# Performance work log

Measured on AMD Instinct MI355X. Metric: run time of the kernel, lower is better.

Reference implementation:

```python
import jax, jax.numpy as jnp
import numpy as np

N_NODES = 50000
N_EDGES = 800000
IN_F, HID, OUT, FC_OUT = 192, 128, 64, 192


def setup_inputs() -> dict:
    key = jax.random.key(0)
    ks = jax.random.split(key, 12)
    s = 0.05
    return {
        "x": jax.random.normal(ks[0], (N_NODES, IN_F), dtype=jnp.float32),
        "edge_index": jax.random.randint(ks[1], (2, N_EDGES), 0, N_NODES, dtype=jnp.int64),
        "W1": jax.random.normal(ks[2], (IN_F, HID), dtype=jnp.float32) * s,
        "b1": jnp.zeros((HID,), jnp.float32),
        "Wg": jax.random.normal(ks[3], (HID, HID), dtype=jnp.float32) * s,
        "a_src": jax.random.normal(ks[4], (HID,), dtype=jnp.float32) * s,
        "a_dst": jax.random.normal(ks[5], (HID,), dtype=jnp.float32) * s,
        "bg": jnp.zeros((HID,), jnp.float32),
        "W2": jax.random.normal(ks[6], (HID, OUT), dtype=jnp.float32) * s,
        "b2": jnp.zeros((OUT,), jnp.float32),
        "Wf": jax.random.normal(ks[7], (OUT, FC_OUT), dtype=jnp.float32) * s,
        "bf": jnp.zeros((FC_OUT,), jnp.float32),
    }


def reference(x, edge_index, W1, b1, Wg, a_src, a_dst, bg, W2, b2, Wf, bf):
    N = x.shape[0]
    loops = jnp.arange(N, dtype=edge_index.dtype)
    src = jnp.concatenate([edge_index[0], loops])  # [E+N]
    dst = jnp.concatenate([edge_index[1], loops])

    # GCN symmetric normalization with self-loops (PyG gcn_norm)
    deg = jax.ops.segment_sum(jnp.ones_like(dst, dtype=x.dtype), dst, num_segments=N)
    dinv = jax.lax.rsqrt(jnp.maximum(deg, 1.0))  # deg >= 1 due to self-loops
    norm = dinv[src] * dinv[dst]  # [E+N]

    def gcn(h, W, b):
        h = h @ W
        out = jax.ops.segment_sum(h[src] * norm[:, None], dst, num_segments=N)
        return out + b

    h = gcn(x, W1, b1)  # [N, HID]

    # GAT layer (1 head, PyG defaults: self-loops, LeakyReLU(0.2), softmax over dst)
    hg = h @ Wg
    al = hg @ a_src  # [N]
    ar = hg @ a_dst  # [N]
    e = jax.nn.leaky_relu(al[src] + ar[dst], 0.2)  # [E+N]
    emax = jax.ops.segment_max(e, dst, num_segments=N)
    ex = jnp.exp(e - emax[dst])
    denom = jax.ops.segment_sum(ex, dst, num_segments=N)
    alpha = ex / denom[dst]
    h = jax.ops.segment_sum(hg[src] * alpha[:, None], dst, num_segments=N) + bg

    h = jax.nn.relu(h)
    h = gcn(h, W2, b2)  # [N, OUT]
    return h @ Wf + bf  # [N, 192]
```

## Files before the change

### kernel.cpp

```cpp
#include <hip/hip_runtime.h>
#include <hip/hip_fp16.h>
#include <cstdint>
#include <cstddef>

#define NN 50000
#define NE 800000
#define RNG 8
#define RSZ ((NN + RNG - 1) / RNG)
#define CPR 256
#define FILLB (RNG*CPR)

typedef _Float16 half8 __attribute__((ext_vector_type(8)));
typedef float    f32x4 __attribute__((ext_vector_type(4)));

static __device__ __forceinline__ float lrelu02(float x){ return x > 0.f ? x : 0.2f*x; }

static __device__ __forceinline__ float2 h2f(uint32_t u){
  __half2 h = *reinterpret_cast<__half2*>(&u);
  return __half22float2(h);
}
static __device__ __forceinline__ uint32_t f2h(float a, float b){
  __half2 h = __floats2half2_rn(a, b);
  return *reinterpret_cast<uint32_t*>(&h);
}
static __device__ __forceinline__ void acc8p(float* acc, uint4 raw, float p){
  float2 f0=h2f(raw.x), f1=h2f(raw.y), f2=h2f(raw.z), f3=h2f(raw.w);
  acc[0]+=p*f0.x; acc[1]+=p*f0.y; acc[2]+=p*f1.x; acc[3]+=p*f1.y;
  acc[4]+=p*f2.x; acc[5]+=p*f2.y; acc[6]+=p*f3.x; acc[7]+=p*f3.y;
}
static __device__ __forceinline__ void acc8s(float* acc, uint4 raw){
  float2 f0=h2f(raw.x), f1=h2f(raw.y), f2=h2f(raw.z), f3=h2f(raw.w);
  acc[0]+=f0.x; acc[1]+=f0.y; acc[2]+=f1.x; acc[3]+=f1.y;
  acc[4]+=f2.x; acc[5]+=f2.y; acc[6]+=f3.x; acc[7]+=f3.y;
}

__global__ __launch_bounds__(256) void pack_all_kernel(
    const float* __restrict__ W1, const float* __restrict__ Wg,
    const float* __restrict__ W2, const float* __restrict__ Wf,
    _Float16* __restrict__ B1, _Float16* __restrict__ B2,
    _Float16* __restrict__ B3, _Float16* __restrict__ B4,
    int* __restrict__ cnt)
{
  const int b = blockIdx.x;
  if (b >= 240){
    const int i = (b - 240)*256 + threadIdx.x;
    if (i < NN) cnt[i] = 0;
    return;
  }
  const float* B; _Float16* O; int K, N, base;
  if      (b < 96)  { B = W1; O = B1; K = 192; N = 128; base = 0;   }
  else if (b < 160) { B = Wg; O = B2; K = 128; N = 128; base = 96;  }
  else if (b < 192) { B = W2; O = B3; K = 128; N = 64;  base = 160; }
  else              { B = Wf; O = B4; K = 64;  N = 192; base = 192; }
  const int i = (b - base)*256 + threadIdx.x;
  if (i >= K*N) return;
  const int j    = i & 7;
  const int lane = (i >> 3) & 63;
  const int tile = i >> 9;
  const int ntl  = N >> 4;
  const int ct   = tile % ntl;
  const int k0   = (tile / ntl) << 5;
  const int k = k0 + ((lane >> 4) << 3) + j;
  const int n = (ct << 4) + (lane & 15);
  O[i] = (_Float16)B[(size_t)k*N + n];
}

__global__ __launch_bounds__(256) void count_kernel(const int* __restrict__ dst,
                                                    int* __restrict__ cnt, int E){
  const int r  = blockIdx.x % RNG;
  const int i  = blockIdx.x / RNG;
  const int lo = r * RSZ;
  const int hi = min(lo + RSZ, NN);
  const int cs = (E + CPR - 1) / CPR;
  const int e1 = min((i+1)*cs, E);
  for (int e = i*cs + threadIdx.x; e < e1; e += 256){
    const int d = dst[e];
    if (d >= lo && d < hi) atomicAdd(&cnt[d], 1);
  }
}

__global__ __launch_bounds__(1024) void scan1_kernel(const int* __restrict__ cnt,
      int* __restrict__ incl, int* __restrict__ bsum, int N){
  __shared__ int tmp[1024];
  const int t = threadIdx.x;
  const int i = blockIdx.x*1024 + t;
  int v = (i < N) ? cnt[i] : 0;
  tmp[t] = v;
  __syncthreads();
  #pragma unroll
  for (int off = 1; off < 1024; off <<= 1){
    int u = (t >= off) ? tmp[t-off] : 0;
    __syncthreads();
    tmp[t] += u;
    __syncthreads();
  }
  if (i < N) incl[i] = tmp[t];
  if (t == 1023) bsum[blockIdx.x] = tmp[t];
}

__global__ __launch_bounds__(256) void scan3_kernel(const int* __restrict__ cnt,
      const int* __restrict__ incl, const int* __restrict__ bsum,
      int* __restrict__ rp, int* __restrict__ fillp,
      float* __restrict__ dinv, int N, int NB){
  __shared__ int pre[64];
  const int t = threadIdx.x;
  if (t < 64){
    int own = (t < NB) ? bsum[t] : 0;
    int v = own;
    #pragma unroll
    for (int off = 1; off < 64; off <<= 1){
      int u = __shfl_up(v, off, 64);
      if (t >= off) v += u;
    }
    pre[t] = v - own;
  }
  __syncthreads();
  const int i = blockIdx.x*256 + t;
  if (i >= N) return;
  const int c = cnt[i];
  const int e = pre[i >> 10] + incl[i] - c;
  rp[i] = e; fillp[i] = e;
  dinv[i] = rsqrtf((float)(c + 1));
  if (i == N-1) rp[N] = e + c;
}

template<int K, int NT, bool AHALF, bool HALF_OUT, bool DOTS>
static __device__ __forceinline__ void gemm_block(
    const void* __restrict__ Av, const _Float16* __restrict__ Bsw,
    const float* __restrict__ bias, const float* __restrict__ rowscale,
    const float* __restrict__ avs, const float* __restrict__ avd,
    float* __restrict__ al, float* __restrict__ ar,
    void* __restrict__ Cv, int M, int N, int bm, int t)
{
  constexpr int NTL = NT*4;
  const int w    = t >> 6;
  const int lane = t & 63;
  const int m    = lane & 15;
  const int quad = lane >> 4;

  f32x4 acc[NTL];
  #pragma unroll
  for (int ct = 0; ct < NTL; ++ct) acc[ct] = (f32x4){0.f,0.f,0.f,0.f};

  const int row = bm + w*16 + m;
  const _Float16* bp = Bsw + lane*8;

  #pragma unroll
  for (int k0 = 0; k0 < K; k0 += 32){
    union { half8 h; uint4 u; uint32_t w[4]; } ua;
    if constexpr (AHALF){
      if (row < M){
        ua.u = *(const uint4*)((const _Float16*)Av + (size_t)row*K + k0 + quad*8);
      } else {
        ua.u = make_uint4(0u,0u,0u,0u);
      }
    } else {
      if (row < M){
        const float* Arow = (const float*)Av + (size_t)row*K;
        const float4 va = *(const float4*)(Arow + k0 + quad*8);
        const float4 vb = *(const float4*)(Arow + k0 + quad*8 + 4);
        ua.w[0] = f2h(va.x, va.y);
        ua.w[1] = f2h(va.z, va.w);
        ua.w[2] = f2h(vb.x, vb.y);
        ua.w[3] = f2h(vb.z, vb.w);
      } else {
        ua.u = make_uint4(0u,0u,0u,0u);
      }
    }
    const half8 af = ua.h;
    #pragma unroll
    for (int ct = 0; ct < NTL; ++ct){
      const half8 bf = *(const half8*)(bp + ((size_t)((k0>>5)*NTL + ct))*512);
      acc[ct] = __builtin_amdgcn_mfma_f32_16x16x32_f16(af, bf, acc[ct], 0, 0, 0);
    }
  }

  float rs[4];
  #pragma unroll
  for (int reg = 0; reg < 4; ++reg){
    const int r = bm + w*16 + quad*4 + reg;
    rs[reg] = (rowscale && r < M) ? rowscale[r] : 1.f;
  }
  float dal[4] = {0.f,0.f,0.f,0.f};
  float dar[4] = {0.f,0.f,0.f,0.f};
  #pragma unroll
  for (int ct = 0; ct < NTL; ++ct){
    const int colg = ct*16 + m;
    const float bv = bias ? bias[colg] : 0.f;
    float s_c = 0.f, d_c = 0.f;
    if constexpr (DOTS){ s_c = avs[colg]; d_c = avd[colg]; }
    #pragma unroll
    for (int reg = 0; reg < 4; ++reg){
      const int r = bm + w*16 + quad*4 + reg;
      if (r < M){
        const float v = rs[reg]*acc[ct][reg] + bv;
        if constexpr (DOTS){ dal[reg] += v*s_c; dar[reg] += v*d_c; }
        if constexpr (HALF_OUT){
          ((__half*)Cv)[(size_t)r*N + colg] = __float2half(v);
        } else {
          ((float*)Cv)[(size_t)r*N + colg] = v;
        }
      }
    }
  }
  if constexpr (DOTS){
    #pragma unroll
    for (int off = 1; off < 16; off <<= 1){
      #pragma unroll
      for (int reg = 0; reg < 4; ++reg){
        dal[reg] += __shfl_xor(dal[reg], off, 64);
        dar[reg] += __shfl_xor(dar[reg], off, 64);
      }
    }
    if (m == 0){
      #pragma unroll
      for (int reg = 0; reg < 4; ++reg){
        const int r = bm + w*16 + quad*4 + reg;
        if (r < M){
          al[r] = dal[reg];
          ar[r] = dar[reg];
        }
      }
    }
  }
}

template<int K, int NT, bool AHALF, bool HALF_OUT, bool DOTS>
__global__ __launch_bounds__(256) void gemm_mfma_kernel(
    const void* __restrict__ Av, const _Float16* __restrict__ Bsw,
    const float* __restrict__ bias, const float* __restrict__ rowscale,
    const float* __restrict__ avs, const float* __restrict__ avd,
    float* __restrict__ al, float* __restrict__ ar,
    void* __restrict__ Cv, int M, int N)
{
  gemm_block<K,NT,AHALF,HALF_OUT,DOTS>(Av, Bsw, bias, rowscale, avs, avd, al, ar,
                                       Cv, M, N, blockIdx.x*64, threadIdx.x);
}

__global__ __launch_bounds__(256) void fill_gemm1_kernel(
    const int* __restrict__ src, const int* __restrict__ dst,
    int* __restrict__ fillp, int* __restrict__ col, int E,
    const float* __restrict__ A, const _Float16* __restrict__ B1,
    const float* __restrict__ dinv, __half* __restrict__ C, int M)
{
  if (blockIdx.x < FILLB){
    const int r  = blockIdx.x % RNG;
    const int i  = blockIdx.x / RNG;
    const int lo = r * RSZ;
    const int hi = min(lo + RSZ, NN);
    const int cs = (E + CPR - 1) / CPR;
    const int e1 = min((i+1)*cs, E);
    for (int e = i*cs + threadIdx.x; e < e1; e += 256){
      const int d = dst[e];
      if (d >= lo && d < hi){
        const int s = src[e];
        const int pos = atomicAdd(&fillp[d], 1);
        col[pos] = s;
      }
    }
    return;
  }
  const int bm = (blockIdx.x - FILLB) * 64;
  gemm_block<192,2,false,true,false>(A, B1, nullptr, dinv, nullptr, nullptr,
                                     nullptr, nullptr, C, M, 128, bm, threadIdx.x);
}

__global__ __launch_bounds__(256) void gcn_agg128_kernel(
    const __half* __restrict__ H, const int* __restrict__ rp, const int* __restrict__ col,
    const float* __restrict__ dinv, const float* __restrict__ bias,
    __half* __restrict__ out, int N)
{
  const int t  = threadIdx.x;
  const int n  = blockIdx.x * 16 + (t >> 4);
  const int gl = t & 15;
  if (n >= N) return;
  const float dn = dinv[n];
  float acc[8];
  {
    uint4 raw = *(const uint4*)(H + (size_t)n*128 + gl*8);
    float2 f0=h2f(raw.x), f1=h2f(raw.y), f2=h2f(raw.z), f3=h2f(raw.w);
    acc[0]=f0.x; acc[1]=f0.y; acc[2]=f1.x; acc[3]=f1.y;
    acc[4]=f2.x; acc[5]=f2.y; acc[6]=f3.x; acc[7]=f3.y;
  }
  const int s0 = rp[n], s1 = rp[n+1];
  for (int c0 = s0; c0 < s1; c0 += 16){
    const int nc = min(16, s1 - c0);
    int sl = (gl < nc) ? col[c0 + gl] : 0;
    #pragma unroll 2
    for (int j = 0; j < nc; ++j){
      const int s = __shfl(sl, j, 16);
      acc8s(acc, *(const uint4*)(H + (size_t)s*128 + gl*8));
    }
  }
  const float* bp = bias + gl*8;
  float4 b0 = *(const float4*)(bp);
  float4 b1 = *(const float4*)(bp + 4);
  uint4 o;
  o.x = f2h(dn*acc[0] + b0.x, dn*acc[1] + b0.y);
  o.y = f2h(dn*acc[2] + b0.z, dn*acc[3] + b0.w);
  o.z = f2h(dn*acc[4] + b1.x, dn*acc[5] + b1.y);
  o.w = f2h(dn*acc[6] + b1.z, dn*acc[7] + b1.w);
  *(uint4*)(out + (size_t)n*128 + gl*8) = o;
}

__global__ __launch_bounds__(256) void gcn_agg64_kernel(
    const __half* __restrict__ H, const int* __restrict__ rp, const int* __restrict__ col,
    const float* __restrict__ dinv, const float* __restrict__ bias,
    __half* __restrict__ out, int N)
{
  const int t  = threadIdx.x;
  const int n  = blockIdx.x * 32 + (t >> 3);
  const int gl = t & 7;
  if (n >= N) return;
  const float dn = dinv[n];
  float acc[8];
  {
    uint4 raw = *(const uint4*)(H + (size_t)n*64 + gl*8);
    float2 f0=h2f(raw.x), f1=h2f(raw.y), f2=h2f(raw.z), f3=h2f(raw.w);
    acc[0]=f0.x; acc[1]=f0.y; acc[2]=f1.x; acc[3]=f1.y;
    acc[4]=f2.x; acc[5]=f2.y; acc[6]=f3.x; acc[7]=f3.y;
  }
  const int s0 = rp[n], s1 = rp[n+1];
  for (int c0 = s0; c0 < s1; c0 += 8){
    const int nc = min(8, s1 - c0);
    int sl = (gl < nc) ? col[c0 + gl] : 0;
    #pragma unroll 2
    for (int j = 0; j < nc; ++j){
      const int s = __shfl(sl, j, 8);
      acc8s(acc, *(const uint4*)(H + (size_t)s*64 + gl*8));
    }
  }
  const float* bp = bias + gl*8;
  float4 b0 = *(const float4*)(bp);
  float4 b1 = *(const float4*)(bp + 4);
  uint4 o;
  o.x = f2h(dn*acc[0] + b0.x, dn*acc[1] + b0.y);
  o.y = f2h(dn*acc[2] + b0.z, dn*acc[3] + b0.w);
  o.z = f2h(dn*acc[4] + b1.x, dn*acc[5] + b1.y);
  o.w = f2h(dn*acc[6] + b1.z, dn*acc[7] + b1.w);
  *(uint4*)(out + (size_t)n*64 + gl*8) = o;
}

__global__ __launch_bounds__(256) void gat_agg_kernel(
    const __half* __restrict__ HG, const int* __restrict__ rp, const int* __restrict__ col,
    const float* __restrict__ al, const float* __restrict__ ar,
    const float* __restrict__ bias, __half* __restrict__ out, int N)
{
  const int t  = threadIdx.x;
  const int n  = blockIdx.x * 16 + (t >> 4);
  const int gl = t & 15;
  if (n >= N) return;
  const float arn = ar[n];
  const float pself = __expf(lrelu02(al[n] + arn));
  float lpart = 0.f;
  float acc[8];
  {
    uint4 raw = *(const uint4*)(HG + (size_t)n*128 + gl*8);
    float2 f0=h2f(raw.x), f1=h2f(raw.y), f2=h2f(raw.z), f3=h2f(raw.w);
    acc[0]=pself*f0.x; acc[1]=pself*f0.y; acc[2]=pself*f1.x; acc[3]=pself*f1.y;
    acc[4]=pself*f2.x; acc[5]=pself*f2.y; acc[6]=pself*f3.x; acc[7]=pself*f3.y;
  }
  const int s0 = rp[n], s1 = rp[n+1];
  for (int c0 = s0; c0 < s1; c0 += 16){
    const int nc = min(16, s1 - c0);
    int   sl = (gl < nc) ? col[c0 + gl] : 0;
    float pl = (gl < nc) ? __expf(lrelu02(al[sl] + arn)) : 0.f;
    lpart += pl;
    #pragma unroll 2
    for (int j = 0; j < nc; ++j){
      const int   s = __shfl(sl, j, 16);
      const float p = __shfl(pl, j, 16);
      acc8p(acc, *(const uint4*)(HG + (size_t)s*128 + gl*8), p);
    }
  }
  #pragma unroll
  for (int off = 8; off > 0; off >>= 1) lpart += __shfl_xor(lpart, off, 16);
  const float inv = 1.f / (pself + lpart);
  const float* bp = bias + gl*8;
  float4 b0 = *(const float4*)(bp);
  float4 b1 = *(const float4*)(bp + 4);
  uint4 o;
  o.x = f2h(fmaxf(acc[0]*inv + b0.x, 0.f), fmaxf(acc[1]*inv + b0.y, 0.f));
  o.y = f2h(fmaxf(acc[2]*inv + b0.z, 0.f), fmaxf(acc[3]*inv + b0.w, 0.f));
  o.z = f2h(fmaxf(acc[4]*inv + b1.x, 0.f), fmaxf(acc[5]*inv + b1.y, 0.f));
  o.w = f2h(fmaxf(acc[6]*inv + b1.z, 0.f), fmaxf(acc[7]*inv + b1.w, 0.f));
  *(uint4*)(out + (size_t)n*128 + gl*8) = o;
}

extern "C" void kernel_launch(void* const* d_in, const int* in_sizes, int n_in,
                              void* d_out, int out_size, void* d_ws, size_t ws_size,
                              hipStream_t stream)
{
  const float* x     = (const float*)d_in[0];
  const int*   ei    = (const int*)d_in[1];
  const float* W1    = (const float*)d_in[2];
  const float* b1    = (const float*)d_in[3];
  const float* Wg    = (const float*)d_in[4];
  const float* a_src = (const float*)d_in[5];
  const float* a_dst = (const float*)d_in[6];
  const float* bg    = (const float*)d_in[7];
  const float* W2    = (const float*)d_in[8];
  const float* b2    = (const float*)d_in[9];
  const float* Wf    = (const float*)d_in[10];
  const float* bf    = (const float*)d_in[11];
  const int N = NN, E = NE;
  const int* src = ei;
  const int* dst = ei + E;

  char* p = (char*)d_ws;
  auto alloc = [&](size_t bytes)->char*{
    char* r = p; p += (bytes + 511) & ~size_t(511); return r;
  };
  int*      cnt   = (int*)     alloc((size_t)N*4);
  int*      incl  = (int*)     alloc((size_t)N*4);
  int*      bsum  = (int*)     alloc(64*4);
  int*      rp    = (int*)     alloc((size_t)(N+1)*4);
  int*      fillp = (int*)     alloc((size_t)N*4);
  int*      col   = (int*)     alloc((size_t)E*4);
  float*    dinv  = (float*)   alloc((size_t)N*4);
  float*    alar_ = (float*)   alloc((size_t)N*8);
  __half*   H16   = (__half*)  alloc((size_t)N*128*2);
  __half*   Hb    = (__half*)  alloc((size_t)N*128*2);
  _Float16* B1    = (_Float16*)alloc(24576*2);
  _Float16* B2    = (_Float16*)alloc(16384*2);
  _Float16* B3    = (_Float16*)alloc(8192*2);
  _Float16* B4    = (_Float16*)alloc(12288*2);
  float*    al    = alar_;
  float*    ar    = alar_ + N;

  const int NB = (N + 1023) / 1024;
  const int gm  = (N + 63) / 64;
  const int g16 = (N + 15) / 16;
  const int g32 = (N + 31) / 32;

  pack_all_kernel<<<240 + (NN + 255)/256, 256, 0, stream>>>(
      W1, Wg, W2, Wf, B1, B2, B3, B4, cnt);
  count_kernel<<<FILLB, 256, 0, stream>>>(dst, cnt, E);
  scan1_kernel<<<NB, 1024, 0, stream>>>(cnt, incl, bsum, N);
  scan3_kernel<<<(N+255)/256, 256, 0, stream>>>(cnt, incl, bsum, rp, fillp, dinv, N, NB);

  fill_gemm1_kernel<<<FILLB + gm, 256, 0, stream>>>(
      src, dst, fillp, col, E, x, B1, dinv, H16, N);

  gcn_agg128_kernel<<<g16, 256, 0, stream>>>(H16, rp, col, dinv, b1, Hb, N);
  gemm_mfma_kernel<128,2,true,true,true><<<gm, 256, 0, stream>>>(
      Hb, B2, nullptr, nullptr, a_src, a_dst, al, ar, H16, N, 128);
  gat_agg_kernel<<<g16, 256, 0, stream>>>(H16, rp, col, al, ar, bg, Hb, N);
  gemm_mfma_kernel<128,1,true,true,false><<<gm, 256, 0, stream>>>(
      Hb, B3, nullptr, dinv, nullptr, nullptr, nullptr, nullptr, H16, N, 64);
  gcn_agg64_kernel<<<g32, 256, 0, stream>>>(H16, rp, col, dinv, b2, Hb, N);
  gemm_mfma_kernel<64,3,true,false,false><<<gm, 256, 0, stream>>>(
      Hb, B4, bf, nullptr, nullptr, nullptr, nullptr, nullptr, d_out, N, 192);
}
```

Baseline: 322.9 us.

## Overlap first GEMM with degree counting and apply source norm during aggregation

The first GEMM now runs fused with the degree-count pass instead of with the CSR fill, so it no longer needs dinv and can overlap the count atomics. Because the row scale is no longer applied inside the GEMM, the first GCN aggregation gathers dinv[src] per neighbor and multiplies by it there, pre-scaling the self term by dinv[n]. The count and fill loops are unrolled by four to issue more independent loads per thread, and the count pass uses half as many chunks per range. The cost is an extra per-edge dinv gather and shuffle in the aggregation, and a standalone fill kernel launch.

```diff
diff --git a/kernel.cpp b/kernel.cpp
--- a/kernel.cpp
+++ b/kernel.cpp
@@ -7,8 +7,10 @@
 #define NE 800000
 #define RNG 8
 #define RSZ ((NN + RNG - 1) / RNG)
-#define CPR 256
-#define FILLB (RNG*CPR)
+#define CNT_CPR 128
+#define CNTB (RNG*CNT_CPR)
+#define FIL_CPR 256
+#define FILB (RNG*FIL_CPR)
 
 typedef _Float16 half8 __attribute__((ext_vector_type(8)));
 typedef float    f32x4 __attribute__((ext_vector_type(4)));
@@ -65,20 +67,6 @@
   O[i] = (_Float16)B[(size_t)k*N + n];
 }
 
-__global__ __launch_bounds__(256) void count_kernel(const int* __restrict__ dst,
-                                                    int* __restrict__ cnt, int E){
-  const int r  = blockIdx.x % RNG;
-  const int i  = blockIdx.x / RNG;
-  const int lo = r * RSZ;
-  const int hi = min(lo + RSZ, NN);
-  const int cs = (E + CPR - 1) / CPR;
-  const int e1 = min((i+1)*cs, E);
-  for (int e = i*cs + threadIdx.x; e < e1; e += 256){
-    const int d = dst[e];
-    if (d >= lo && d < hi) atomicAdd(&cnt[d], 1);
-  }
-}
-
 __global__ __launch_bounds__(1024) void scan1_kernel(const int* __restrict__ cnt,
       int* __restrict__ incl, int* __restrict__ bsum, int N){
   __shared__ int tmp[1024];
@@ -122,6 +110,32 @@
   rp[i] = e; fillp[i] = e;
   dinv[i] = rsqrtf((float)(c + 1));
   if (i == N-1) rp[N] = e + c;
+}
+
+__global__ __launch_bounds__(256) void fill_kernel(const int* __restrict__ src,
+      const int* __restrict__ dst, int* __restrict__ fillp,
+      int* __restrict__ col, int E){
+  const int r  = blockIdx.x % RNG;
+  const int i  = blockIdx.x / RNG;
+  const int lo = r * RSZ;
+  const int hi = min(lo + RSZ, NN);
+  const int cs = (E + FIL_CPR - 1) / FIL_CPR;
+  const int e1 = min((i+1)*cs, E);
+  int e = i*cs + threadIdx.x;
+  for (; e + 768 < e1; e += 1024){
+    const int d0 = dst[e];       const int d1 = dst[e+256];
+    const int d2 = dst[e+512];   const int d3 = dst[e+768];
+    const int s0 = src[e];       const int s1 = src[e+256];
+    const int s2 = src[e+512];   const int s3 = src[e+768];
+    if (d0 >= lo && d0 < hi){ col[atomicAdd(&fillp[d0],1)] = s0; }
+    if (d1 >= lo && d1 < hi){ col[atomicAdd(&fillp[d1],1)] = s1; }
+    if (d2 >= lo && d2 < hi){ col[atomicAdd(&fillp[d2],1)] = s2; }
+    if (d3 >= lo && d3 < hi){ col[atomicAdd(&fillp[d3],1)] = s3; }
+  }
+  for (; e < e1; e += 256){
+    const int d = dst[e];
+    if (d >= lo && d < hi){ col[atomicAdd(&fillp[d],1)] = src[e]; }
+  }
 }
 
 template<int K, int NT, bool AHALF, bool HALF_OUT, bool DOTS>
@@ -237,35 +251,39 @@
                                        Cv, M, N, blockIdx.x*64, threadIdx.x);
 }
 
-__global__ __launch_bounds__(256) void fill_gemm1_kernel(
-    const int* __restrict__ src, const int* __restrict__ dst,
-    int* __restrict__ fillp, int* __restrict__ col, int E,
+__global__ __launch_bounds__(256) void count_gemm1_kernel(
+    const int* __restrict__ dst, int* __restrict__ cnt, int E,
     const float* __restrict__ A, const _Float16* __restrict__ B1,
-    const float* __restrict__ dinv, __half* __restrict__ C, int M)
-{
-  if (blockIdx.x < FILLB){
+    __half* __restrict__ C, int M)
+{
+  if (blockIdx.x < CNTB){
     const int r  = blockIdx.x % RNG;
     const int i  = blockIdx.x / RNG;
     const int lo = r * RSZ;
     const int hi = min(lo + RSZ, NN);
-    const int cs = (E + CPR - 1) / CPR;
+    const int cs = (E + CNT_CPR - 1) / CNT_CPR;
     const int e1 = min((i+1)*cs, E);
-    for (int e = i*cs + threadIdx.x; e < e1; e += 256){
+    int e = i*cs + threadIdx.x;
+    for (; e + 768 < e1; e += 1024){
+      const int d0 = dst[e];       const int d1 = dst[e+256];
+      const int d2 = dst[e+512];   const int d3 = dst[e+768];
+      if (d0 >= lo && d0 < hi) atomicAdd(&cnt[d0], 1);
+      if (d1 >= lo && d1 < hi) atomicAdd(&cnt[d1], 1);
+      if (d2 >= lo && d2 < hi) atomicAdd(&cnt[d2], 1);
+      if (d3 >= lo && d3 < hi) atomicAdd(&cnt[d3], 1);
+    }
+    for (; e < e1; e += 256){
       const int d = dst[e];
-      if (d >= lo && d < hi){
-        const int s = src[e];
-        const int pos = atomicAdd(&fillp[d], 1);
-        col[pos] = s;
-      }
+      if (d >= lo && d < hi) atomicAdd(&cnt[d], 1);
     }
     return;
   }
-  const int bm = (blockIdx.x - FILLB) * 64;
-  gemm_block<192,2,false,true,false>(A, B1, nullptr, dinv, nullptr, nullptr,
+  const int bm = (blockIdx.x - CNTB) * 64;
+  gemm_block<192,2,false,true,false>(A, B1, nullptr, nullptr, nullptr, nullptr,
                                      nullptr, nullptr, C, M, 128, bm, threadIdx.x);
 }
 
-__global__ __launch_bounds__(256) void gcn_agg128_kernel(
+__global__ __launch_bounds__(256) void gcn_agg128d_kernel(
     const __half* __restrict__ H, const int* __restrict__ rp, const int* __restrict__ col,
     const float* __restrict__ dinv, const float* __restrict__ bias,
     __half* __restrict__ out, int N)
@@ -279,17 +297,19 @@
   {
     uint4 raw = *(const uint4*)(H + (size_t)n*128 + gl*8);
     float2 f0=h2f(raw.x), f1=h2f(raw.y), f2=h2f(raw.z), f3=h2f(raw.w);
-    acc[0]=f0.x; acc[1]=f0.y; acc[2]=f1.x; acc[3]=f1.y;
-    acc[4]=f2.x; acc[5]=f2.y; acc[6]=f3.x; acc[7]=f3.y;
+    acc[0]=dn*f0.x; acc[1]=dn*f0.y; acc[2]=dn*f1.x; acc[3]=dn*f1.y;
+    acc[4]=dn*f2.x; acc[5]=dn*f2.y; acc[6]=dn*f3.x; acc[7]=dn*f3.y;
   }
   const int s0 = rp[n], s1 = rp[n+1];
   for (int c0 = s0; c0 < s1; c0 += 16){
     const int nc = min(16, s1 - c0);
-    int sl = (gl < nc) ? col[c0 + gl] : 0;
+    int   sl = (gl < nc) ? col[c0 + gl] : 0;
+    float dl = (gl < nc) ? dinv[sl] : 0.f;
     #pragma unroll 2
     for (int j = 0; j < nc; ++j){
-      const int s = __shfl(sl, j, 16);
-      acc8s(acc, *(const uint4*)(H + (size_t)s*128 + gl*8));
+      const int   s = __shfl(sl, j, 16);
+      const float p = __shfl(dl, j, 16);
+      acc8p(acc, *(const uint4*)(H + (size_t)s*128 + gl*8), p);
     }
   }
   const float* bp = bias + gl*8;
@@ -428,21 +448,21 @@
   float*    al    = alar_;
   float*    ar    = alar_ + N;
 
-  const int NB = (N + 1023) / 1024;
+  const int NB  = (N + 1023) / 1024;
   const int gm  = (N + 63) / 64;
   const int g16 = (N + 15) / 16;
   const int g32 = (N + 31) / 32;
 
   pack_all_kernel<<<240 + (NN + 255)/256, 256, 0, stream>>>(
       W1, Wg, W2, Wf, B1, B2, B3, B4, cnt);
-  count_kernel<<<FILLB, 256, 0, stream>>>(dst, cnt, E);
+
+  count_gemm1_kernel<<<CNTB + gm, 256, 0, stream>>>(dst, cnt, E, x, B1, H16, N);
+
   scan1_kernel<<<NB, 1024, 0, stream>>>(cnt, incl, bsum, N);
   scan3_kernel<<<(N+255)/256, 256, 0, stream>>>(cnt, incl, bsum, rp, fillp, dinv, N, NB);
-
-  fill_gemm1_kernel<<<FILLB + gm, 256, 0, stream>>>(
-      src, dst, fillp, col, E, x, B1, dinv, H16, N);
-
-  gcn_agg128_kernel<<<g16, 256, 0, stream>>>(H16, rp, col, dinv, b1, Hb, N);
+  fill_kernel<<<FILB, 256, 0, stream>>>(src, dst, fillp, col, E);
+
+  gcn_agg128d_kernel<<<g16, 256, 0, stream>>>(H16, rp, col, dinv, b1, Hb, N);
   gemm_mfma_kernel<128,2,true,true,true><<<gm, 256, 0, stream>>>(
       Hb, B2, nullptr, nullptr, a_src, a_dst, al, ar, H16, N, 128);
   gat_agg_kernel<<<g16, 256, 0, stream>>>(H16, rp, col, al, ar, bg, Hb, N);
```

Result: no change. 325.9 us (+0.9%).
